# Kernel tuning notes

Measured on AMD Instinct MI355X. Metric: run time of the kernel, lower is better.

Reference implementation:

```python
import jax, jax.numpy as jnp
import numpy as np

B, N, D = 4, 2048, 512
H, HD = 8, 64  # heads, output_dim per head


def setup_inputs() -> dict:
    key = jax.random.key(0)
    ks = jax.random.split(key, 6)
    x = jax.random.normal(ks[0], (B, N, D), dtype=jnp.float32)
    adj = (jax.random.uniform(ks[1], (N, N)) < 0.1).astype(jnp.float32)
    adj = jnp.maximum(adj, jnp.eye(N, dtype=jnp.float32))
    s = 0.02
    Wq = jax.random.normal(ks[2], (D, H * HD), dtype=jnp.float32) * s
    Wk = jax.random.normal(ks[3], (D, H * HD), dtype=jnp.float32) * s
    Wv = jax.random.normal(ks[4], (D, H * HD), dtype=jnp.float32) * s
    bq = jnp.zeros((H * HD,), dtype=jnp.float32)
    bk = jnp.zeros((H * HD,), dtype=jnp.float32)
    bv = jnp.zeros((H * HD,), dtype=jnp.float32)
    return {"x": x, "adj": adj, "Wq": Wq, "bq": bq, "Wk": Wk, "bk": bk, "Wv": Wv, "bv": bv}


def reference(x, adj, Wq, bq, Wk, bk, Wv, bv):
    b, n, _ = x.shape
    q = (x @ Wq + bq).reshape(b, n, H, HD)
    k = (x @ Wk + bk).reshape(b, n, H, HD)
    v = (x @ Wv + bv).reshape(b, n, H, HD)
    # scores: [b, h, i, j]
    scores = jnp.einsum('bihd,bjhd->bhij', q, k) / jnp.sqrt(jnp.float32(HD))
    mask = jnp.where(adj == 0, jnp.float32(-1e9), jnp.float32(0.0))  # [n, n]
    scores = scores + mask[None, None, :, :]
    weights = jax.nn.softmax(scores, axis=-1)
    # dropout is identity at inference (training=False)
    out = jnp.einsum('bhij,bjhd->bihd', weights, v)
    return out.reshape(b, n, H * HD)
```

## Files before the change

kernel.cpp:

```cpp
#include <hip/hip_runtime.h>
#include <hip/hip_bf16.h>
#include <stdint.h>

#define NTOK 2048
#define DIN  512
#define QSCALE 0.18033688011112042f

typedef __attribute__((ext_vector_type(8))) short bf16x8;
typedef __attribute__((ext_vector_type(4))) short bf16x4;
typedef __attribute__((ext_vector_type(4))) float f32x4;

#define MFMA16(a, b, c) __builtin_amdgcn_mfma_f32_16x16x32_bf16((a), (b), (c), 0, 0, 0)

static __device__ __forceinline__ short f2bf(float f) {
  union { float f; uint32_t u; } v; v.f = f;
  uint32_t r = (v.u + 0x7FFFu + ((v.u >> 16) & 1u)) >> 16;
  return (short)r;
}

__global__ __launch_bounds__(256) void k_xbf(const float* __restrict__ x, short* __restrict__ xb) {
  size_t i = (size_t)blockIdx.x * 256 + threadIdx.x;
  const float4 v = *(const float4*)(x + i * 4);
  bf16x4 h;
  h[0] = f2bf(v.x); h[1] = f2bf(v.y); h[2] = f2bf(v.z); h[3] = f2bf(v.w);
  *(bf16x4*)(xb + i * 4) = h;
}

__global__ __launch_bounds__(256) void k_wt(const float* __restrict__ W, short* __restrict__ Wt) {
  __shared__ float tile[32][33];
  int bo = blockIdx.x * 32, bc = blockIdx.y * 32;
  int tx = threadIdx.x & 31, ty = threadIdx.x >> 5;
#pragma unroll
  for (int q = 0; q < 4; ++q)
    tile[ty + q * 8][tx] = W[(bc + ty + q * 8) * DIN + bo + tx];
  __syncthreads();
#pragma unroll
  for (int q = 0; q < 4; ++q)
    Wt[(bo + ty + q * 8) * DIN + bc + tx] = f2bf(tile[tx][ty + q * 8]);
}

__global__ __launch_bounds__(256) void k_mask(const float* __restrict__ adj,
                                              unsigned long long* __restrict__ m64) {
  int wid = ((blockIdx.x * blockDim.x + threadIdx.x) >> 6);
  int lane = threadIdx.x & 63;
  int i = wid >> 5, wd = wid & 31;
  float a = adj[i * NTOK + wd * 64 + lane];
  unsigned long long b = __ballot(a != 0.0f);
  if (lane == 0) m64[i * 32 + wd] = b;
}

__global__ __launch_bounds__(256) void k_qkv(const short* __restrict__ xb,
                                             const short* __restrict__ Wt,
                                             const float* __restrict__ bq,
                                             const float* __restrict__ bk,
                                             const float* __restrict__ bv,
                                             short* __restrict__ Qb, short* __restrict__ Kb,
                                             short* __restrict__ Vb) {
  __shared__ short As[128 * 40];
  __shared__ short Bs[128 * 40];
  const int z = blockIdx.z;
  const short* Wz = Wt + z * DIN * DIN;
  const float* bias = (z == 0) ? bq : ((z == 1) ? bk : bv);
  const int mbase = blockIdx.x * 128, nbase = blockIdx.y * 128;
  const int tid = threadIdx.x;
  const int lane = tid & 63, w = tid >> 6;
  const int wr = w >> 1, wc = w & 1;
  const int lrow = lane & 15, lgrp = lane >> 4;

  f32x4 acc[4][4];
#pragma unroll
  for (int a = 0; a < 4; ++a)
#pragma unroll
    for (int b = 0; b < 4; ++b) acc[a][b] = (f32x4){0.f, 0.f, 0.f, 0.f};

  for (int kb = 0; kb < DIN; kb += 32) {
#pragma unroll
    for (int t = 0; t < 2; ++t) {
      int idx = tid + t * 256;
      int r = idx >> 2, c8 = idx & 3;
      *(bf16x8*)(As + r * 40 + c8 * 8) =
          *(const bf16x8*)(xb + (size_t)(mbase + r) * DIN + kb + c8 * 8);
    }
#pragma unroll
    for (int t = 0; t < 2; ++t) {
      int idx = tid + t * 256;
      int r = idx >> 2, c8 = idx & 3;
      *(bf16x8*)(Bs + r * 40 + c8 * 8) =
          *(const bf16x8*)(Wz + (size_t)(nbase + r) * DIN + kb + c8 * 8);
    }
    __syncthreads();
    bf16x8 af[4], bf[4];
#pragma unroll
    for (int mi = 0; mi < 4; ++mi)
      af[mi] = *(bf16x8*)(As + (wr * 64 + mi * 16 + lrow) * 40 + lgrp * 8);
#pragma unroll
    for (int ni = 0; ni < 4; ++ni)
      bf[ni] = *(bf16x8*)(Bs + (wc * 64 + ni * 16 + lrow) * 40 + lgrp * 8);
#pragma unroll
    for (int mi = 0; mi < 4; ++mi)
#pragma unroll
      for (int ni = 0; ni < 4; ++ni) acc[mi][ni] = MFMA16(af[mi], bf[ni], acc[mi][ni]);
    __syncthreads();
  }

#pragma unroll
  for (int ni = 0; ni < 4; ++ni) {
    int go = nbase + wc * 64 + ni * 16 + lrow;
    float bv_ = bias[go];
    int h = go >> 6, d = go & 63;
#pragma unroll
    for (int mi = 0; mi < 4; ++mi) {
#pragma unroll
      for (int v = 0; v < 4; ++v) {
        int gm = mbase + wr * 64 + mi * 16 + lgrp * 4 + v;
        int b = gm >> 11, n = gm & 2047;
        int bh = b * 8 + h;
        float val = acc[mi][ni][v] + bv_;
        if (z == 0)
          Qb[(size_t)bh * (NTOK * 64) + n * 64 + d] = f2bf(val * QSCALE);
        else if (z == 1)
          Kb[(size_t)bh * (NTOK * 64) + n * 64 + d] = f2bf(val);
        else
          Vb[(size_t)bh * (64 * NTOK) + d * NTOK + n] = f2bf(val);
      }
    }
  }
}

__global__ __launch_bounds__(256) void k_attn(const short* __restrict__ Qb,
                                              const short* __restrict__ Kb,
                                              const short* __restrict__ Vb,
                                              const unsigned long long* __restrict__ m64,
                                              float* __restrict__ out) {
  __shared__ short Kl[64 * 72];
  __shared__ short Vl[64 * 72];
  __shared__ short Pl[4][16 * 72];
  const int itile = blockIdx.x, bh = blockIdx.y;
  const int ibase = itile * 64;
  const int tid = threadIdx.x, lane = tid & 63, w = tid >> 6;
  const int lrow = lane & 15, lgrp = lane >> 4;

  const short* Qp = Qb + (size_t)bh * (NTOK * 64);
  const short* Kp = Kb + (size_t)bh * (NTOK * 64);
  const short* Vp = Vb + (size_t)bh * (64 * NTOK);

  const int qrow = ibase + w * 16 + lrow;
  bf16x8 qa[2];
  qa[0] = *(const bf16x8*)(Qp + (size_t)qrow * 64 + lgrp * 8);
  qa[1] = *(const bf16x8*)(Qp + (size_t)qrow * 64 + 32 + lgrp * 8);

  const unsigned long long* mword = m64 + (size_t)qrow * 32;

  f32x4 oacc[4];
#pragma unroll
  for (int dn = 0; dn < 4; ++dn) oacc[dn] = (f32x4){0.f, 0.f, 0.f, 0.f};
  float lrun = 0.f;

  for (int jt = 0; jt < 32; ++jt) {
    const int jbase = jt * 64;
#pragma unroll
    for (int idx = tid; idx < 512; idx += 256) {
      int r = idx >> 3, s = idx & 7;
      *(bf16x8*)(Kl + r * 72 + s * 8) = *(const bf16x8*)(Kp + (size_t)(jbase + r) * 64 + s * 8);
      *(bf16x8*)(Vl + r * 72 + s * 8) = *(const bf16x8*)(Vp + (size_t)r * NTOK + jbase + s * 8);
    }
    __syncthreads();

    f32x4 sf[4];
#pragma unroll
    for (int jn = 0; jn < 4; ++jn) {
      f32x4 zz = (f32x4){0.f, 0.f, 0.f, 0.f};
      zz = MFMA16(*(bf16x8*)(Kl + (jn * 16 + lrow) * 72 + lgrp * 8), qa[0], zz);
      zz = MFMA16(*(bf16x8*)(Kl + (jn * 16 + lrow) * 72 + 32 + lgrp * 8), qa[1], zz);
      sf[jn] = zz;
    }

    unsigned long long wrd = mword[jt];
    uint32_t lo = ((uint32_t)wrd) >> (lgrp * 4);
    uint32_t hi = ((uint32_t)(wrd >> 32)) >> (lgrp * 4);
    float p[4][4];
    float ls = 0.f;
#pragma unroll
    for (int jn = 0; jn < 4; ++jn) {
      uint32_t bits = (jn < 2) ? lo : hi;
      const int sh = (jn & 1) * 16;
#pragma unroll
      for (int r = 0; r < 4; ++r) {
        float e = exp2f(sf[jn][r]);
        p[jn][r] = ((bits >> (sh + r)) & 1u) ? e : 0.f;
        ls += p[jn][r];
      }
    }
    lrun += ls;

#pragma unroll
    for (int jn = 0; jn < 4; ++jn) {
      uint32_t w0, w1;
      asm("v_cvt_pk_bf16_f32 %0, %1, %2" : "=v"(w0) : "v"(p[jn][0]), "v"(p[jn][1]));
      asm("v_cvt_pk_bf16_f32 %0, %1, %2" : "=v"(w1) : "v"(p[jn][2]), "v"(p[jn][3]));
      uint2 pk;
      pk.x = w0;
      pk.y = w1;
      *(uint2*)(Pl[w] + lrow * 72 + jn * 16 + lgrp * 4) = pk;
    }

#pragma unroll
    for (int dn = 0; dn < 4; ++dn) {
#pragma unroll
      for (int ks = 0; ks < 2; ++ks) {
        oacc[dn] = MFMA16(*(bf16x8*)(Pl[w] + lrow * 72 + ks * 32 + lgrp * 8),
                          *(bf16x8*)(Vl + (dn * 16 + lrow) * 72 + ks * 32 + lgrp * 8),
                          oacc[dn]);
      }
    }
    __syncthreads();
  }

  float lfull = lrun;
  lfull += __shfl_xor(lfull, 16);
  lfull += __shfl_xor(lfull, 32);

  const int b = bh >> 3, h = bh & 7;
#pragma unroll
  for (int v = 0; v < 4; ++v) {
    float li = __shfl(lfull, lgrp * 4 + v);
    float inv = 1.0f / li;
    int i = ibase + w * 16 + lgrp * 4 + v;
#pragma unroll
    for (int dn = 0; dn < 4; ++dn)
      out[(size_t)(b * NTOK + i) * DIN + h * 64 + dn * 16 + lrow] = oacc[dn][v] * inv;
  }
}

extern "C" void kernel_launch(void* const* d_in, const int* in_sizes, int n_in,
                              void* d_out, int out_size, void* d_ws, size_t ws_size,
                              hipStream_t stream) {
  const float* x   = (const float*)d_in[0];
  const float* adj = (const float*)d_in[1];
  const float* Wq  = (const float*)d_in[2];
  const float* bq  = (const float*)d_in[3];
  const float* Wk  = (const float*)d_in[4];
  const float* bk  = (const float*)d_in[5];
  const float* Wv  = (const float*)d_in[6];
  const float* bv  = (const float*)d_in[7];
  float* out = (float*)d_out;

  char* ws = (char*)d_ws;
  short* Qb = (short*)(ws);
  short* Kb = (short*)(ws + (8u << 20));
  short* Vb = (short*)(ws + (16u << 20));
  short* Wt = (short*)(ws + (24u << 20));
  unsigned long long* m64 = (unsigned long long*)(ws + (26u << 20));
  short* xb = (short*)d_out;

  k_xbf<<<4096, 256, 0, stream>>>(x, xb);
  k_wt<<<dim3(16, 16), 256, 0, stream>>>(Wq, Wt);
  k_wt<<<dim3(16, 16), 256, 0, stream>>>(Wk, Wt + 262144);
  k_wt<<<dim3(16, 16), 256, 0, stream>>>(Wv, Wt + 524288);
  k_mask<<<16384, 256, 0, stream>>>(adj, m64);
  k_qkv<<<dim3(64, 4, 3), 256, 0, stream>>>(xb, Wt, bq, bk, bv, Qb, Kb, Vb);
  k_attn<<<dim3(32, 32), 256, 0, stream>>>(Qb, Kb, Vb, m64, out);
}
```

Baseline: 136.2 us.

## Split attention key range across waves and reduce partial outputs in LDS

```diff
diff --git a/kernel.cpp b/kernel.cpp
--- a/kernel.cpp
+++ b/kernel.cpp
@@ -11,6 +11,8 @@
 typedef __attribute__((ext_vector_type(4))) float f32x4;
 
 #define MFMA16(a, b, c) __builtin_amdgcn_mfma_f32_16x16x32_bf16((a), (b), (c), 0, 0, 0)
+
+union u4bf8 { uint4 u; bf16x8 h; };
 
 static __device__ __forceinline__ short f2bf(float f) {
   union { float f; uint32_t u; } v; v.f = f;
@@ -132,9 +134,8 @@
                                               const short* __restrict__ Vb,
                                               const unsigned long long* __restrict__ m64,
                                               float* __restrict__ out) {
-  __shared__ short Kl[64 * 72];
-  __shared__ short Vl[64 * 72];
-  __shared__ short Pl[4][16 * 72];
+  __shared__ f32x4 red[2048];
+  __shared__ float lred[256];
   const int itile = blockIdx.x, bh = blockIdx.y;
   const int ibase = itile * 64;
   const int tid = threadIdx.x, lane = tid & 63, w = tid >> 6;
@@ -144,91 +145,120 @@
   const short* Kp = Kb + (size_t)bh * (NTOK * 64);
   const short* Vp = Vb + (size_t)bh * (64 * NTOK);
 
-  const int qrow = ibase + w * 16 + lrow;
-  bf16x8 qa[2];
-  qa[0] = *(const bf16x8*)(Qp + (size_t)qrow * 64 + lgrp * 8);
-  qa[1] = *(const bf16x8*)(Qp + (size_t)qrow * 64 + 32 + lgrp * 8);
-
-  const unsigned long long* mword = m64 + (size_t)qrow * 32;
-
-  f32x4 oacc[4];
-#pragma unroll
-  for (int dn = 0; dn < 4; ++dn) oacc[dn] = (f32x4){0.f, 0.f, 0.f, 0.f};
-  float lrun = 0.f;
-
-  for (int jt = 0; jt < 32; ++jt) {
-    const int jbase = jt * 64;
-#pragma unroll
-    for (int idx = tid; idx < 512; idx += 256) {
-      int r = idx >> 3, s = idx & 7;
-      *(bf16x8*)(Kl + r * 72 + s * 8) = *(const bf16x8*)(Kp + (size_t)(jbase + r) * 64 + s * 8);
-      *(bf16x8*)(Vl + r * 72 + s * 8) = *(const bf16x8*)(Vp + (size_t)r * NTOK + jbase + s * 8);
-    }
-    __syncthreads();
-
-    f32x4 sf[4];
-#pragma unroll
-    for (int jn = 0; jn < 4; ++jn) {
-      f32x4 zz = (f32x4){0.f, 0.f, 0.f, 0.f};
-      zz = MFMA16(*(bf16x8*)(Kl + (jn * 16 + lrow) * 72 + lgrp * 8), qa[0], zz);
-      zz = MFMA16(*(bf16x8*)(Kl + (jn * 16 + lrow) * 72 + 32 + lgrp * 8), qa[1], zz);
-      sf[jn] = zz;
-    }
-
-    unsigned long long wrd = mword[jt];
-    uint32_t lo = ((uint32_t)wrd) >> (lgrp * 4);
-    uint32_t hi = ((uint32_t)(wrd >> 32)) >> (lgrp * 4);
-    float p[4][4];
-    float ls = 0.f;
-#pragma unroll
-    for (int jn = 0; jn < 4; ++jn) {
-      uint32_t bits = (jn < 2) ? lo : hi;
-      const int sh = (jn & 1) * 16;
-#pragma unroll
-      for (int r = 0; r < 4; ++r) {
-        float e = exp2f(sf[jn][r]);
-        p[jn][r] = ((bits >> (sh + r)) & 1u) ? e : 0.f;
-        ls += p[jn][r];
-      }
-    }
-    lrun += ls;
-
-#pragma unroll
-    for (int jn = 0; jn < 4; ++jn) {
-      uint32_t w0, w1;
-      asm("v_cvt_pk_bf16_f32 %0, %1, %2" : "=v"(w0) : "v"(p[jn][0]), "v"(p[jn][1]));
-      asm("v_cvt_pk_bf16_f32 %0, %1, %2" : "=v"(w1) : "v"(p[jn][2]), "v"(p[jn][3]));
-      uint2 pk;
-      pk.x = w0;
-      pk.y = w1;
-      *(uint2*)(Pl[w] + lrow * 72 + jn * 16 + lgrp * 4) = pk;
-    }
-
+  bf16x8 qf[4][2];
+#pragma unroll
+  for (int ig = 0; ig < 4; ++ig) {
+    const size_t qr = (size_t)(ibase + ig * 16 + lrow) * 64;
+    qf[ig][0] = *(const bf16x8*)(Qp + qr + lgrp * 8);
+    qf[ig][1] = *(const bf16x8*)(Qp + qr + 32 + lgrp * 8);
+  }
+
+  const unsigned long long* mbase = m64 + (size_t)(ibase + lrow) * 32;
+  const int sh = w * 16 + lgrp * 4;
+
+  f32x4 oacc[4][4];
+#pragma unroll
+  for (int ig = 0; ig < 4; ++ig)
+#pragma unroll
+    for (int dn = 0; dn < 4; ++dn) oacc[ig][dn] = (f32x4){0.f, 0.f, 0.f, 0.f};
+  float lrun[4] = {0.f, 0.f, 0.f, 0.f};
+
+  for (int jp = 0; jp < 16; ++jp) {
+    uint32_t pk[4][4];
+#pragma unroll
+    for (int half = 0; half < 2; ++half) {
+      const int jt = jp * 2 + half;
+      const size_t kr = (size_t)(jt * 64 + w * 16 + lrow) * 64;
+      bf16x8 kf0 = *(const bf16x8*)(Kp + kr + lgrp * 8);
+      bf16x8 kf1 = *(const bf16x8*)(Kp + kr + 32 + lgrp * 8);
+      f32x4 sa[4];
+#pragma unroll
+      for (int ig = 0; ig < 4; ++ig) {
+        f32x4 zz = (f32x4){0.f, 0.f, 0.f, 0.f};
+        zz = MFMA16(kf0, qf[ig][0], zz);
+        zz = MFMA16(kf1, qf[ig][1], zz);
+        sa[ig] = zz;
+      }
+#pragma unroll
+      for (int ig = 0; ig < 4; ++ig) {
+        const uint32_t bits = (uint32_t)(mbase[ig * 512 + jt] >> sh);
+        float p0 = (bits & 1u) ? exp2f(sa[ig][0]) : 0.f;
+        float p1 = (bits & 2u) ? exp2f(sa[ig][1]) : 0.f;
+        float p2 = (bits & 4u) ? exp2f(sa[ig][2]) : 0.f;
+        float p3 = (bits & 8u) ? exp2f(sa[ig][3]) : 0.f;
+        lrun[ig] += (p0 + p1) + (p2 + p3);
+        uint32_t w0, w1;
+        asm("v_cvt_pk_bf16_f32 %0, %1, %2" : "=v"(w0) : "v"(p0), "v"(p1));
+        asm("v_cvt_pk_bf16_f32 %0, %1, %2" : "=v"(w1) : "v"(p2), "v"(p3));
+        pk[ig][half * 2] = w0;
+        pk[ig][half * 2 + 1] = w1;
+      }
+    }
 #pragma unroll
     for (int dn = 0; dn < 4; ++dn) {
-#pragma unroll
-      for (int ks = 0; ks < 2; ++ks) {
-        oacc[dn] = MFMA16(*(bf16x8*)(Pl[w] + lrow * 72 + ks * 32 + lgrp * 8),
-                          *(bf16x8*)(Vl + (dn * 16 + lrow) * 72 + ks * 32 + lgrp * 8),
-                          oacc[dn]);
-      }
-    }
-    __syncthreads();
-  }
-
-  float lfull = lrun;
-  lfull += __shfl_xor(lfull, 16);
-  lfull += __shfl_xor(lfull, 32);
+      const size_t vr = (size_t)(dn * 16 + lrow) * NTOK + jp * 128 + w * 16 + lgrp * 4;
+      const uint2 v0 = *(const uint2*)(Vp + vr);
+      const uint2 v1 = *(const uint2*)(Vp + vr + 64);
+      u4bf8 vb;
+      vb.u = (uint4){v0.x, v0.y, v1.x, v1.y};
+#pragma unroll
+      for (int ig = 0; ig < 4; ++ig) {
+        u4bf8 pa;
+        pa.u = (uint4){pk[ig][0], pk[ig][1], pk[ig][2], pk[ig][3]};
+        oacc[ig][dn] = MFMA16(pa.h, vb.h, oacc[ig][dn]);
+      }
+    }
+  }
+
+  float lr[4];
+#pragma unroll
+  for (int ig = 0; ig < 4; ++ig) {
+    float s = lrun[ig];
+    s += __shfl_xor(s, 16);
+    s += __shfl_xor(s, 32);
+    lr[ig] = s;
+  }
+  if (lane < 16) {
+#pragma unroll
+    for (int ig = 0; ig < 4; ++ig) lred[(ig * 16 + lane) * 4 + w] = lr[ig];
+  }
+#pragma unroll
+  for (int ig = 0; ig < 4; ++ig)
+#pragma unroll
+    for (int c = 0; c < 2; ++c) red[((w * 4 + ig) * 2 + c) * 64 + lane] = oacc[ig][c];
+  __syncthreads();
+
+  float inv[4];
+#pragma unroll
+  for (int v = 0; v < 4; ++v) {
+    const f32x4 t = *(const f32x4*)&lred[(w * 16 + lgrp * 4 + v) * 4];
+    inv[v] = 1.0f / ((t[0] + t[1]) + (t[2] + t[3]));
+  }
 
   const int b = bh >> 3, h = bh & 7;
-#pragma unroll
-  for (int v = 0; v < 4; ++v) {
-    float li = __shfl(lfull, lgrp * 4 + v);
-    float inv = 1.0f / li;
-    int i = ibase + w * 16 + lgrp * 4 + v;
-#pragma unroll
-    for (int dn = 0; dn < 4; ++dn)
-      out[(size_t)(b * NTOK + i) * DIN + h * 64 + dn * 16 + lrow] = oacc[dn][v] * inv;
+  const size_t obase = (size_t)(b * NTOK + ibase + w * 16 + lgrp * 4) * DIN + h * 64 + lrow;
+
+#pragma unroll
+  for (int c = 0; c < 2; ++c) {
+    f32x4 s = red[((0 * 4 + w) * 2 + c) * 64 + lane];
+#pragma unroll
+    for (int wp = 1; wp < 4; ++wp) s += red[((wp * 4 + w) * 2 + c) * 64 + lane];
+#pragma unroll
+    for (int v = 0; v < 4; ++v) out[obase + (size_t)v * DIN + c * 16] = s[v] * inv[v];
+  }
+  __syncthreads();
+#pragma unroll
+  for (int ig = 0; ig < 4; ++ig)
+#pragma unroll
+    for (int c = 0; c < 2; ++c) red[((w * 4 + ig) * 2 + c) * 64 + lane] = oacc[ig][2 + c];
+  __syncthreads();
+#pragma unroll
+  for (int c = 0; c < 2; ++c) {
+    f32x4 s = red[((0 * 4 + w) * 2 + c) * 64 + lane];
+#pragma unroll
+    for (int wp = 1; wp < 4; ++wp) s += red[((wp * 4 + w) * 2 + c) * 64 + lane];
+#pragma unroll
+    for (int v = 0; v < 4; ++v) out[obase + (size_t)v * DIN + (2 + c) * 16] = s[v] * inv[v];
   }
 }
 
```

Result: slower. 207.4 us (+52.3%).

## Fuse adjacency mask into attention as additive bias and prefetch K/V tiles

Applied to the files above, without the earlier changes.

```diff
diff --git a/kernel.cpp b/kernel.cpp
--- a/kernel.cpp
+++ b/kernel.cpp
@@ -37,16 +37,6 @@
 #pragma unroll
   for (int q = 0; q < 4; ++q)
     Wt[(bo + ty + q * 8) * DIN + bc + tx] = f2bf(tile[tx][ty + q * 8]);
-}
-
-__global__ __launch_bounds__(256) void k_mask(const float* __restrict__ adj,
-                                              unsigned long long* __restrict__ m64) {
-  int wid = ((blockIdx.x * blockDim.x + threadIdx.x) >> 6);
-  int lane = threadIdx.x & 63;
-  int i = wid >> 5, wd = wid & 31;
-  float a = adj[i * NTOK + wd * 64 + lane];
-  unsigned long long b = __ballot(a != 0.0f);
-  if (lane == 0) m64[i * 32 + wd] = b;
 }
 
 __global__ __launch_bounds__(256) void k_qkv(const short* __restrict__ xb,
@@ -130,7 +120,7 @@
 __global__ __launch_bounds__(256) void k_attn(const short* __restrict__ Qb,
                                               const short* __restrict__ Kb,
                                               const short* __restrict__ Vb,
-                                              const unsigned long long* __restrict__ m64,
+                                              const float* __restrict__ adj,
                                               float* __restrict__ out) {
   __shared__ short Kl[64 * 72];
   __shared__ short Vl[64 * 72];
@@ -149,60 +139,79 @@
   qa[0] = *(const bf16x8*)(Qp + (size_t)qrow * 64 + lgrp * 8);
   qa[1] = *(const bf16x8*)(Qp + (size_t)qrow * 64 + 32 + lgrp * 8);
 
-  const unsigned long long* mword = m64 + (size_t)qrow * 32;
+  const float* arow = adj + (size_t)qrow * NTOK;
+
+  const int r0 = tid >> 3, s0 = tid & 7;
 
   f32x4 oacc[4];
 #pragma unroll
   for (int dn = 0; dn < 4; ++dn) oacc[dn] = (f32x4){0.f, 0.f, 0.f, 0.f};
   float lrun = 0.f;
 
+  uint4 pfK[2], pfV[2];
+  {
+    const size_t kb0 = (size_t)r0 * 64 + s0 * 8;
+    pfK[0] = *(const uint4*)(Kp + kb0);
+    pfK[1] = *(const uint4*)(Kp + kb0 + 32 * 64);
+    const size_t vb0 = (size_t)r0 * NTOK + s0 * 8;
+    pfV[0] = *(const uint4*)(Vp + vb0);
+    pfV[1] = *(const uint4*)(Vp + vb0 + 32 * NTOK);
+  }
+
   for (int jt = 0; jt < 32; ++jt) {
     const int jbase = jt * 64;
-#pragma unroll
-    for (int idx = tid; idx < 512; idx += 256) {
-      int r = idx >> 3, s = idx & 7;
-      *(bf16x8*)(Kl + r * 72 + s * 8) = *(const bf16x8*)(Kp + (size_t)(jbase + r) * 64 + s * 8);
-      *(bf16x8*)(Vl + r * 72 + s * 8) = *(const bf16x8*)(Vp + (size_t)r * NTOK + jbase + s * 8);
-    }
-    __syncthreads();
-
-    f32x4 sf[4];
+    __syncthreads();
+    *(uint4*)(Kl + r0 * 72 + s0 * 8) = pfK[0];
+    *(uint4*)(Kl + (r0 + 32) * 72 + s0 * 8) = pfK[1];
+    *(uint4*)(Vl + r0 * 72 + s0 * 8) = pfV[0];
+    *(uint4*)(Vl + (r0 + 32) * 72 + s0 * 8) = pfV[1];
+    __syncthreads();
+    if (jt < 31) {
+      const int jn = jbase + 64;
+      const size_t kb1 = (size_t)(jn + r0) * 64 + s0 * 8;
+      pfK[0] = *(const uint4*)(Kp + kb1);
+      pfK[1] = *(const uint4*)(Kp + kb1 + 32 * 64);
+      const size_t vb1 = (size_t)r0 * NTOK + jn + s0 * 8;
+      pfV[0] = *(const uint4*)(Vp + vb1);
+      pfV[1] = *(const uint4*)(Vp + vb1 + 32 * NTOK);
+    }
+    float4 av[4];
+#pragma unroll
+    for (int jn = 0; jn < 4; ++jn)
+      av[jn] = *(const float4*)(arow + jbase + jn * 16 + lgrp * 4);
+
+    f32x4 sa[4];
 #pragma unroll
     for (int jn = 0; jn < 4; ++jn) {
-      f32x4 zz = (f32x4){0.f, 0.f, 0.f, 0.f};
-      zz = MFMA16(*(bf16x8*)(Kl + (jn * 16 + lrow) * 72 + lgrp * 8), qa[0], zz);
-      zz = MFMA16(*(bf16x8*)(Kl + (jn * 16 + lrow) * 72 + 32 + lgrp * 8), qa[1], zz);
-      sf[jn] = zz;
-    }
-
-    unsigned long long wrd = mword[jt];
-    uint32_t lo = ((uint32_t)wrd) >> (lgrp * 4);
-    uint32_t hi = ((uint32_t)(wrd >> 32)) >> (lgrp * 4);
-    float p[4][4];
-    float ls = 0.f;
+      bf16x8 kf0 = *(bf16x8*)(Kl + (jn * 16 + lrow) * 72 + lgrp * 8);
+      bf16x8 kf1 = *(bf16x8*)(Kl + (jn * 16 + lrow) * 72 + 32 + lgrp * 8);
+      f32x4 zz;
+      zz[0] = __builtin_fmaf(av[jn].x, 300.f, -300.f);
+      zz[1] = __builtin_fmaf(av[jn].y, 300.f, -300.f);
+      zz[2] = __builtin_fmaf(av[jn].z, 300.f, -300.f);
+      zz[3] = __builtin_fmaf(av[jn].w, 300.f, -300.f);
+      zz = MFMA16(kf0, qa[0], zz);
+      zz = MFMA16(kf1, qa[1], zz);
+      sa[jn] = zz;
+    }
+
+    float lacc = 0.f;
 #pragma unroll
     for (int jn = 0; jn < 4; ++jn) {
-      uint32_t bits = (jn < 2) ? lo : hi;
-      const int sh = (jn & 1) * 16;
-#pragma unroll
-      for (int r = 0; r < 4; ++r) {
-        float e = exp2f(sf[jn][r]);
-        p[jn][r] = ((bits >> (sh + r)) & 1u) ? e : 0.f;
-        ls += p[jn][r];
-      }
-    }
-    lrun += ls;
-
-#pragma unroll
-    for (int jn = 0; jn < 4; ++jn) {
+      float p0 = exp2f(sa[jn][0]);
+      float p1 = exp2f(sa[jn][1]);
+      float p2 = exp2f(sa[jn][2]);
+      float p3 = exp2f(sa[jn][3]);
+      lacc += (p0 + p1) + (p2 + p3);
       uint32_t w0, w1;
-      asm("v_cvt_pk_bf16_f32 %0, %1, %2" : "=v"(w0) : "v"(p[jn][0]), "v"(p[jn][1]));
-      asm("v_cvt_pk_bf16_f32 %0, %1, %2" : "=v"(w1) : "v"(p[jn][2]), "v"(p[jn][3]));
+      asm("v_cvt_pk_bf16_f32 %0, %1, %2" : "=v"(w0) : "v"(p0), "v"(p1));
+      asm("v_cvt_pk_bf16_f32 %0, %1, %2" : "=v"(w1) : "v"(p2), "v"(p3));
       uint2 pk;
       pk.x = w0;
       pk.y = w1;
       *(uint2*)(Pl[w] + lrow * 72 + jn * 16 + lgrp * 4) = pk;
     }
+    lrun += lacc;
 
 #pragma unroll
     for (int dn = 0; dn < 4; ++dn) {
@@ -213,7 +222,6 @@
                           oacc[dn]);
       }
     }
-    __syncthreads();
   }
 
   float lfull = lrun;
@@ -250,14 +258,12 @@
   short* Kb = (short*)(ws + (8u << 20));
   short* Vb = (short*)(ws + (16u << 20));
   short* Wt = (short*)(ws + (24u << 20));
-  unsigned long long* m64 = (unsigned long long*)(ws + (26u << 20));
   short* xb = (short*)d_out;
 
   k_xbf<<<4096, 256, 0, stream>>>(x, xb);
   k_wt<<<dim3(16, 16), 256, 0, stream>>>(Wq, Wt);
   k_wt<<<dim3(16, 16), 256, 0, stream>>>(Wk, Wt + 262144);
   k_wt<<<dim3(16, 16), 256, 0, stream>>>(Wv, Wt + 524288);
-  k_mask<<<16384, 256, 0, stream>>>(adj, m64);
   k_qkv<<<dim3(64, 4, 3), 256, 0, stream>>>(xb, Wt, bq, bk, bv, Qb, Kb, Vb);
-  k_attn<<<dim3(32, 32), 256, 0, stream>>>(Qb, Kb, Vb, m64, out);
-}
+  k_attn<<<dim3(32, 32), 256, 0, stream>>>(Qb, Kb, Vb, adj, out);
+}
```

After: 235.3 us. +72.8%, slower.

## Prefetch next K/V tile and mask word into registers during attention compute

Applied to the files above, without the earlier changes.

```diff
diff --git a/kernel.cpp b/kernel.cpp
--- a/kernel.cpp
+++ b/kernel.cpp
@@ -127,11 +127,11 @@
   }
 }
 
-__global__ __launch_bounds__(256) void k_attn(const short* __restrict__ Qb,
-                                              const short* __restrict__ Kb,
-                                              const short* __restrict__ Vb,
-                                              const unsigned long long* __restrict__ m64,
-                                              float* __restrict__ out) {
+__global__ __launch_bounds__(256, 5) void k_attn(const short* __restrict__ Qb,
+                                                 const short* __restrict__ Kb,
+                                                 const short* __restrict__ Vb,
+                                                 const unsigned long long* __restrict__ m64,
+                                                 float* __restrict__ out) {
   __shared__ short Kl[64 * 72];
   __shared__ short Vl[64 * 72];
   __shared__ short Pl[4][16 * 72];
@@ -151,20 +151,34 @@
 
   const unsigned long long* mword = m64 + (size_t)qrow * 32;
 
+  const int r0 = tid >> 3, s0 = tid & 7;
+
   f32x4 oacc[4];
 #pragma unroll
   for (int dn = 0; dn < 4; ++dn) oacc[dn] = (f32x4){0.f, 0.f, 0.f, 0.f};
   float lrun = 0.f;
 
+  uint4 pfK0 = *(const uint4*)(Kp + (size_t)r0 * 64 + s0 * 8);
+  uint4 pfK1 = *(const uint4*)(Kp + (size_t)(r0 + 32) * 64 + s0 * 8);
+  uint4 pfV0 = *(const uint4*)(Vp + (size_t)r0 * NTOK + s0 * 8);
+  uint4 pfV1 = *(const uint4*)(Vp + (size_t)(r0 + 32) * NTOK + s0 * 8);
+  unsigned long long mw = mword[0];
+  *(uint4*)(Kl + r0 * 72 + s0 * 8) = pfK0;
+  *(uint4*)(Kl + (r0 + 32) * 72 + s0 * 8) = pfK1;
+  *(uint4*)(Vl + r0 * 72 + s0 * 8) = pfV0;
+  *(uint4*)(Vl + (r0 + 32) * 72 + s0 * 8) = pfV1;
+  __syncthreads();
+
   for (int jt = 0; jt < 32; ++jt) {
-    const int jbase = jt * 64;
-#pragma unroll
-    for (int idx = tid; idx < 512; idx += 256) {
-      int r = idx >> 3, s = idx & 7;
-      *(bf16x8*)(Kl + r * 72 + s * 8) = *(const bf16x8*)(Kp + (size_t)(jbase + r) * 64 + s * 8);
-      *(bf16x8*)(Vl + r * 72 + s * 8) = *(const bf16x8*)(Vp + (size_t)r * NTOK + jbase + s * 8);
-    }
-    __syncthreads();
+    unsigned long long mw_nxt = 0;
+    if (jt < 31) {
+      const int jn = (jt + 1) * 64;
+      pfK0 = *(const uint4*)(Kp + (size_t)(jn + r0) * 64 + s0 * 8);
+      pfK1 = *(const uint4*)(Kp + (size_t)(jn + r0 + 32) * 64 + s0 * 8);
+      pfV0 = *(const uint4*)(Vp + (size_t)r0 * NTOK + jn + s0 * 8);
+      pfV1 = *(const uint4*)(Vp + (size_t)(r0 + 32) * NTOK + jn + s0 * 8);
+      mw_nxt = mword[jt + 1];
+    }
 
     f32x4 sf[4];
 #pragma unroll
@@ -175,9 +189,8 @@
       sf[jn] = zz;
     }
 
-    unsigned long long wrd = mword[jt];
-    uint32_t lo = ((uint32_t)wrd) >> (lgrp * 4);
-    uint32_t hi = ((uint32_t)(wrd >> 32)) >> (lgrp * 4);
+    uint32_t lo = ((uint32_t)mw) >> (lgrp * 4);
+    uint32_t hi = ((uint32_t)(mw >> 32)) >> (lgrp * 4);
     float p[4][4];
     float ls = 0.f;
 #pragma unroll
@@ -213,7 +226,16 @@
                           oacc[dn]);
       }
     }
-    __syncthreads();
+
+    if (jt < 31) {
+      __syncthreads();
+      *(uint4*)(Kl + r0 * 72 + s0 * 8) = pfK0;
+      *(uint4*)(Kl + (r0 + 32) * 72 + s0 * 8) = pfK1;
+      *(uint4*)(Vl + r0 * 72 + s0 * 8) = pfV0;
+      *(uint4*)(Vl + (r0 + 32) * 72 + s0 * 8) = pfV1;
+      mw = mw_nxt;
+      __syncthreads();
+    }
   }
 
   float lfull = lrun;
```

New measurement: 126.3 us. 1.08x faster.
